# Kernel optimization log

Measured on AMD Instinct MI355X. Metric: run time of the kernel, lower is better.

Reference implementation:

```python
import jax, jax.numpy as jnp
import numpy as np
import math

N = 4096
D = 256
H = 8
DH = D // H
E_RAND = 131072
EPS = 1e-5


def _layernorm(x, g, b):
    mu = jnp.mean(x, axis=-1, keepdims=True)
    var = jnp.mean((x - mu) ** 2, axis=-1, keepdims=True)
    return (x - mu) * jax.lax.rsqrt(var + EPS) * g + b


def setup_inputs() -> dict:
    key = jax.random.key(0)
    ks = jax.random.split(key, 16)
    s = 1.0 / math.sqrt(D)
    x = jax.random.normal(ks[0], (N, D), dtype=jnp.float32)
    src = jax.random.randint(ks[1], (E_RAND,), 0, N)
    dst = jax.random.randint(ks[2], (E_RAND,), 0, N)
    loop = jnp.arange(N)
    edge_index = jnp.stack([jnp.concatenate([src, loop]),
                            jnp.concatenate([dst, loop])]).astype(jnp.int64)
    def lin(k):
        return jax.random.normal(k, (D, D), dtype=jnp.float32) * s
    return {
        "x": x,
        "edge_index": edge_index,
        "Wq": lin(ks[3]), "bq": jnp.zeros((D,), jnp.float32),
        "Wk": lin(ks[4]), "bk": jnp.zeros((D,), jnp.float32),
        "Wv": lin(ks[5]), "bv": jnp.zeros((D,), jnp.float32),
        "Wo": lin(ks[6]), "bo": jnp.zeros((D,), jnp.float32),
        "g1": jnp.ones((D,), jnp.float32), "b1": jnp.zeros((D,), jnp.float32),
        "g2": jnp.ones((D,), jnp.float32), "b2": jnp.zeros((D,), jnp.float32),
        "Wm1": jax.random.normal(ks[7], (D, 2 * D), jnp.float32) * s,
        "bm1": jnp.zeros((2 * D,), jnp.float32),
        "Wm2": jax.random.normal(ks[8], (2 * D, D), jnp.float32) * (1.0 / math.sqrt(2 * D)),
        "bm2": jnp.zeros((D,), jnp.float32),
    }


def reference(x, edge_index, Wq, bq, Wk, bk, Wv, bv, Wo, bo,
              g1, b1, g2, b2, Wm1, bm1, Wm2, bm2):
    scale = 1.0 / math.sqrt(DH)
    h = _layernorm(x, g1, b1)
    # [N, D] -> [H, N, DH]
    q = (h @ Wq + bq).reshape(N, H, DH).transpose(1, 0, 2)
    k = (h @ Wk + bk).reshape(N, H, DH).transpose(1, 0, 2)
    v = (h @ Wv + bv).reshape(N, H, DH).transpose(1, 0, 2)
    att = jnp.einsum('hnd,hmd->hnm', q, k) * scale  # [H, N, N]
    # mask: True everywhere except edges (edge positions are attended)
    mask = jnp.ones((N, N), dtype=bool).at[edge_index[0], edge_index[1]].set(False)
    att = jnp.where(mask[None, :, :], -jnp.inf, att)
    att = jax.nn.softmax(att, axis=-1)
    y = jnp.einsum('hnm,hmd->hnd', att, v)  # [H, N, DH]
    y = y.transpose(1, 0, 2).reshape(N, D)
    x = x + (y @ Wo + bo)
    h2 = _layernorm(x, g2, b2)
    x = x + (jax.nn.gelu(h2 @ Wm1 + bm1, approximate=False) @ Wm2 + bm2)
    return x
```

## Files before the change

kernel.cpp:

```cpp
#include <hip/hip_runtime.h>
#include <hip/hip_bf16.h>

#define N_NODES 4096
#define D_MODEL 256
#define NWORDS 128
#define CAP 256

typedef __attribute__((ext_vector_type(8))) short short8;
typedef __attribute__((ext_vector_type(4))) float f32x4;

__device__ __forceinline__ unsigned short f2b(float f) {
    unsigned u = __float_as_uint(f);
    return (unsigned short)((u + 0x7FFFu + ((u >> 16) & 1u)) >> 16);
}
__device__ __forceinline__ float b2f(unsigned short u) {
    return __uint_as_float((unsigned)u << 16);
}

__global__ __launch_bounds__(256) void prep_kernel(const float* __restrict__ Wq,
        const float* __restrict__ Wk, const float* __restrict__ Wv,
        const float* __restrict__ Wo, const float* __restrict__ Wm1,
        const float* __restrict__ Wm2, unsigned short* __restrict__ wbf,
        uint4* __restrict__ bitmap, const int* __restrict__ ei,
        int* __restrict__ flag, const float* __restrict__ x,
        const float* __restrict__ g1, const float* __restrict__ b1,
        unsigned short* __restrict__ h) {
    int b = blockIdx.x, t = threadIdx.x;
    if (b < 2048) {
        int e = b * 256 + t;
        const float* W; int base, K, M;
        if (e < 262144) {
            int r = e >> 16;
            W = (r == 0) ? Wq : (r == 1) ? Wk : (r == 2) ? Wv : Wo;
            base = r << 16; K = 256; M = 256;
        } else if (e < 393216) { W = Wm1; base = 262144; K = 256; M = 512; }
        else                   { W = Wm2; base = 393216; K = 512; M = 256; }
        int i = e - base;
        int m = i / K, k = i - m * K;
        wbf[e] = f2b(W[k * M + m]);
    } else if (b < 2560) {
        bitmap[(size_t)(b - 2048) * 256 + t] = uint4{0, 0, 0, 0};
    } else if (b == 2560) {
        if (t == 0) {
            int is64 = 1;
            for (int i = 1; i < 128; i += 2)
                if (ei[i] != 0) { is64 = 0; break; }
            *flag = is64;
        }
    } else {
        int row = b - 2561;
        float v = x[row * D_MODEL + t];
        __shared__ float red[4];
        float s = v;
        #pragma unroll
        for (int off = 32; off; off >>= 1) s += __shfl_down(s, off, 64);
        if ((t & 63) == 0) red[t >> 6] = s;
        __syncthreads();
        float mu = (red[0] + red[1] + red[2] + red[3]) * (1.0f / 256.0f);
        __syncthreads();
        float d = v - mu;
        float s2 = d * d;
        #pragma unroll
        for (int off = 32; off; off >>= 1) s2 += __shfl_down(s2, off, 64);
        if ((t & 63) == 0) red[t >> 6] = s2;
        __syncthreads();
        float var = (red[0] + red[1] + red[2] + red[3]) * (1.0f / 256.0f);
        h[row * D_MODEL + t] = f2b(d * rsqrtf(var + 1e-5f) * g1[t] + b1[t]);
    }
}

template <int K, int MODE, bool LNA, bool STATS>
__global__ __launch_bounds__(512) void gemm_bf16(const unsigned short* __restrict__ A,
        const float* __restrict__ Af, const float* __restrict__ psum,
        const float* __restrict__ psum2, const float* __restrict__ lng,
        const float* __restrict__ lnb, const unsigned short* __restrict__ BT,
        const float* __restrict__ bias, const float* __restrict__ bias_k,
        const float* __restrict__ bias_v, const float* __restrict__ R,
        float* __restrict__ Cf, unsigned short* __restrict__ Cb,
        unsigned short* __restrict__ Ck, unsigned short* __restrict__ Cv,
        float* __restrict__ opsum, float* __restrict__ opsum2, int M,
        const int* __restrict__ ei, int E, const int* __restrict__ flag,
        unsigned* __restrict__ bitmap, int nadj) {
    int tid = threadIdx.x;
    if (MODE == 3 && (int)blockIdx.x < nadj) {
        int e = (int)blockIdx.x * 512 + tid;
        if (e < E) {
            int n, m;
            if (*flag) { n = ei[2 * e]; m = ei[2 * (E + e)]; }
            else       { n = ei[e];     m = ei[E + e]; }
            atomicOr(&bitmap[n * NWORDS + (m >> 5)], 1u << (m & 31));
        }
        return;
    }
    __shared__ unsigned short Asm[64][72];
    __shared__ unsigned short Bsm[64][72];
    __shared__ float psA[64][2], psA2[64][2];
    __shared__ float muS[64], invS[64];

    int bx2  = (MODE == 3) ? ((int)blockIdx.x - nadj) : 0;
    int brow = (MODE == 3) ? ((bx2 & 63) << 6) : ((int)blockIdx.x << 6);
    int by   = (MODE == 3) ? (bx2 >> 6) : (int)blockIdx.y;
    int bcol = by << 6;
    int wid = tid >> 6, lane = tid & 63;
    int wr = wid >> 1, wc = wid & 1;
    int l15 = lane & 15, lhi = lane >> 4;
    int r0 = tid >> 3, c0 = (tid & 7) << 3;

    float mu_r = 0.f, inv_r = 0.f;
    if (LNA) {
        if (tid < 64) {
            float4 s4 = ((const float4*)psum)[brow + tid];
            float4 q4 = ((const float4*)psum2)[brow + tid];
            float S  = s4.x + s4.y + s4.z + s4.w;
            float S2 = q4.x + q4.y + q4.z + q4.w;
            float mu = S * (1.0f / 256.0f);
            muS[tid] = mu;
            invS[tid] = rsqrtf(S2 * (1.0f / 256.0f) - mu * mu + 1e-5f);
        }
        __syncthreads();
        mu_r = muS[r0]; inv_r = invS[r0];
    }

    const unsigned short* Bp = BT + (size_t)(bcol + r0) * K + c0;
    f32x4 acc[2] = {};
    short8 areg;
    float4 xa, xb, ga, gb, ba, bb;
    if (LNA) {
        const float* Xp = Af + (size_t)(brow + r0) * 256 + c0;
        xa = *(const float4*)(Xp);
        xb = *(const float4*)(Xp + 4);
        ga = *(const float4*)(lng + c0); gb = *(const float4*)(lng + c0 + 4);
        ba = *(const float4*)(lnb + c0); bb = *(const float4*)(lnb + c0 + 4);
    } else {
        areg = *(const short8*)(A + (size_t)(brow + r0) * K + c0);
    }
    short8 breg = *(const short8*)(Bp);

    #pragma unroll
    for (int k0 = 0; k0 < K; k0 += 64) {
        if (LNA) {
            float xv[8] = {xa.x, xa.y, xa.z, xa.w, xb.x, xb.y, xb.z, xb.w};
            float gv[8] = {ga.x, ga.y, ga.z, ga.w, gb.x, gb.y, gb.z, gb.w};
            float bv[8] = {ba.x, ba.y, ba.z, ba.w, bb.x, bb.y, bb.z, bb.w};
            short8 o;
            #pragma unroll
            for (int j = 0; j < 8; ++j)
                o[j] = (short)f2b((xv[j] - mu_r) * inv_r * gv[j] + bv[j]);
            *(short8*)&Asm[r0][c0] = o;
        } else {
            *(short8*)&Asm[r0][c0] = areg;
        }
        *(short8*)&Bsm[r0][c0] = breg;
        __syncthreads();
        if (k0 + 64 < K) {
            if (LNA) {
                const float* Xp = Af + (size_t)(brow + r0) * 256 + k0 + 64 + c0;
                xa = *(const float4*)(Xp);
                xb = *(const float4*)(Xp + 4);
                ga = *(const float4*)(lng + k0 + 64 + c0);
                gb = *(const float4*)(lng + k0 + 64 + c0 + 4);
                ba = *(const float4*)(lnb + k0 + 64 + c0);
                bb = *(const float4*)(lnb + k0 + 64 + c0 + 4);
            } else {
                areg = *(const short8*)(A + (size_t)(brow + r0) * K + k0 + 64 + c0);
            }
            breg = *(const short8*)(Bp + k0 + 64);
        }
        #pragma unroll
        for (int ks = 0; ks < 2; ++ks) {
            int kc = ks * 32 + lhi * 8;
            short8 a_0 = *(const short8*)&Asm[wr * 16 + l15][kc];
            short8 b_0 = *(const short8*)&Bsm[wc * 32 + l15][kc];
            short8 b_1 = *(const short8*)&Bsm[wc * 32 + 16 + l15][kc];
            acc[0] = __builtin_amdgcn_mfma_f32_16x16x32_bf16(a_0, b_0, acc[0], 0, 0, 0);
            acc[1] = __builtin_amdgcn_mfma_f32_16x16x32_bf16(a_0, b_1, acc[1], 0, 0, 0);
        }
        __syncthreads();
    }

    float cs[2][4];
    #pragma unroll
    for (int sn = 0; sn < 2; ++sn) {
        int col = bcol + wc * 32 + sn * 16 + l15;
        float bs;
        if (MODE == 3)
            bs = (col < 256) ? bias[col]
               : (col < 512) ? bias_k[col - 256] : bias_v[col - 512];
        else
            bs = bias[col];
        #pragma unroll
        for (int r = 0; r < 4; ++r) {
            int row = brow + wr * 16 + lhi * 4 + r;
            float c = acc[sn][r] + bs;
            if (MODE == 1) {
                c = 0.5f * c * (1.0f + erff(c * 0.70710678118654752f));
                Cb[(size_t)row * M + col] = f2b(c);
            } else if (MODE == 2) {
                c += R[(size_t)row * M + col];
                Cf[(size_t)row * M + col] = c;
            } else if (MODE == 3) {
                int part = col >> 8, cc = col & 255;
                unsigned short* dst = (part == 0) ? Cb : (part == 1) ? Ck : Cv;
                dst[(((size_t)(cc >> 5) * N_NODES + row) << 5) + (cc & 31)] = f2b(c);
            } else {
                Cb[(size_t)row * M + col] = f2b(c);
            }
            if (STATS) cs[sn][r] = c;
        }
    }
    if (STATS) {
        #pragma unroll
        for (int r = 0; r < 4; ++r) {
            float s  = cs[0][r] + cs[1][r];
            float s2 = cs[0][r] * cs[0][r] + cs[1][r] * cs[1][r];
            #pragma unroll
            for (int off = 1; off < 16; off <<= 1) {
                s  += __shfl_xor(s, off, 64);
                s2 += __shfl_xor(s2, off, 64);
            }
            if (l15 == 0) {
                int rl = wr * 16 + lhi * 4 + r;
                psA[rl][wc] = s; psA2[rl][wc] = s2;
            }
        }
        __syncthreads();
        if (tid < 64) {
            opsum [(size_t)(brow + tid) * 4 + by] = psA[tid][0] + psA[tid][1];
            opsum2[(size_t)(brow + tid) * 4 + by] = psA2[tid][0] + psA2[tid][1];
        }
    }
}

__global__ __launch_bounds__(256) void attn_kernel(const unsigned short* __restrict__ qh,
        const unsigned short* __restrict__ kh, const unsigned short* __restrict__ vh,
        const unsigned* __restrict__ bitmap, unsigned short* __restrict__ y) {
    int bid = blockIdx.x, tid = threadIdx.x;
    int h = bid & 7, oct = bid >> 3;
    int g = tid >> 5, lane = tid & 31;
    int n = oct * 8 + g;
    __shared__ int sIdx[8][CAP];

    const unsigned short* qp = qh + (((size_t)h * N_NODES + n) << 5);
    float qreg[32];
    #pragma unroll
    for (int i = 0; i < 4; ++i) {
        short8 q8 = *(const short8*)(qp + i * 8);
        #pragma unroll
        for (int j = 0; j < 8; ++j) qreg[i * 8 + j] = b2f((unsigned short)q8[j]);
    }

    uint4 w4 = ((const uint4*)(bitmap + (size_t)n * NWORDS))[lane];
    unsigned words[4] = {w4.x, w4.y, w4.z, w4.w};
    int pc = __popc(w4.x) + __popc(w4.y) + __popc(w4.z) + __popc(w4.w);
    int pre = pc;
    #pragma unroll
    for (int off = 1; off < 32; off <<= 1) {
        int u = __shfl_up(pre, off, 32);
        if (lane >= off) pre += u;
    }
    int c = __shfl(pre, 31, 32);
    int off = pre - pc;
    #pragma unroll
    for (int i = 0; i < 4; ++i) {
        unsigned word = words[i];
        int wbase = ((lane << 2) + i) << 5;
        while (word) {
            int bit = __ffs(word) - 1;
            word &= word - 1;
            if (off < CAP) sIdx[g][off] = wbase + bit;
            ++off;
        }
    }
    c = min(c, CAP);
    __syncthreads();

    const unsigned short* kbase = kh + ((size_t)h * N_NODES << 5);
    const unsigned short* vbase = vh + ((size_t)h * N_NODES << 5) + lane;
    const float sc = 0.17677669529663687f;
    float m_run = -INFINITY, S = 0.0f, acc = 0.0f;
    for (int b0 = 0; b0 < c; b0 += 32) {
        int j = b0 + lane;
        float s = -INFINITY;
        if (j < c) {
            const unsigned short* kp = kbase + ((size_t)sIdx[g][j] << 5);
            float d = 0.0f;
            #pragma unroll
            for (int i = 0; i < 4; ++i) {
                short8 k8 = *(const short8*)(kp + i * 8);
                #pragma unroll
                for (int e = 0; e < 8; ++e)
                    d = fmaf(qreg[i * 8 + e], b2f((unsigned short)k8[e]), d);
            }
            s = d * sc;
        }
        float bm = s;
        #pragma unroll
        for (int off2 = 16; off2; off2 >>= 1) bm = fmaxf(bm, __shfl_xor(bm, off2, 32));
        float newM = fmaxf(m_run, bm);
        float p = (j < c) ? __expf(s - newM) : 0.0f;
        float bs = p;
        #pragma unroll
        for (int off2 = 16; off2; off2 >>= 1) bs += __shfl_xor(bs, off2, 32);
        float scale = __expf(m_run - newM);
        S = S * scale + bs;
        acc *= scale;
        int lim = min(32, c - b0);
        #pragma unroll 4
        for (int jj = 0; jj < lim; ++jj) {
            float pj = __shfl(p, jj, 32);
            int m = sIdx[g][b0 + jj];
            acc = fmaf(pj, b2f(vbase[(size_t)m << 5]), acc);
        }
        m_run = newM;
    }
    y[(size_t)n * 256 + h * 32 + lane] = f2b(acc / S);
}

extern "C" void kernel_launch(void* const* d_in, const int* in_sizes, int n_in,
                              void* d_out, int out_size, void* d_ws, size_t ws_size,
                              hipStream_t stream) {
    const float* x   = (const float*)d_in[0];
    const int*   ei  = (const int*)d_in[1];
    const float* Wq  = (const float*)d_in[2];  const float* bq  = (const float*)d_in[3];
    const float* Wk  = (const float*)d_in[4];  const float* bk  = (const float*)d_in[5];
    const float* Wv  = (const float*)d_in[6];  const float* bv  = (const float*)d_in[7];
    const float* Wo  = (const float*)d_in[8];  const float* bo  = (const float*)d_in[9];
    const float* g1  = (const float*)d_in[10]; const float* b1  = (const float*)d_in[11];
    const float* g2  = (const float*)d_in[12]; const float* b2  = (const float*)d_in[13];
    const float* Wm1 = (const float*)d_in[14]; const float* bm1 = (const float*)d_in[15];
    const float* Wm2 = (const float*)d_in[16]; const float* bm2 = (const float*)d_in[17];
    float* out = (float*)d_out;
    int E = in_sizes[1] / 2;
    int nadj = (E + 511) / 512;

    char* WS = (char*)d_ws;
    const size_t MB = 1u << 20;
    unsigned*       bitmap = (unsigned*)WS;
    int*            flag   = (int*)(WS + 2 * MB);
    float*          psum   = (float*)(WS + 2 * MB + 4096);
    float*          psum2  = (float*)(WS + 2 * MB + 4096 + 65536);
    unsigned short* wbf    = (unsigned short*)(WS + 3 * MB);
    unsigned short* y      = (unsigned short*)(WS + 4 * MB);
    float*          x1     = (float*)(WS + 6 * MB);
    unsigned short* m1     = (unsigned short*)(WS + 10 * MB);
    unsigned short* h      = (unsigned short*)(WS + 14 * MB);
    unsigned short* qh     = (unsigned short*)(WS + 16 * MB);
    unsigned short* kh     = (unsigned short*)(WS + 18 * MB);
    unsigned short* vh     = (unsigned short*)(WS + 20 * MB);

    const unsigned short* WTqkv = wbf;
    const unsigned short* WTo   = wbf + 196608;
    const unsigned short* WTm1  = wbf + 262144;
    const unsigned short* WTm2  = wbf + 393216;

    prep_kernel<<<6657, 256, 0, stream>>>(Wq, Wk, Wv, Wo, Wm1, Wm2, wbf,
                                          (uint4*)bitmap, ei, flag, x, g1, b1, h);
    gemm_bf16<256, 3, false, false><<<nadj + 768, 512, 0, stream>>>(h, nullptr,
            nullptr, nullptr, nullptr, nullptr, WTqkv, bq, bk, bv, nullptr,
            nullptr, qh, kh, vh, nullptr, nullptr, 768, ei, E, flag, bitmap, nadj);
    attn_kernel<<<N_NODES, 256, 0, stream>>>(qh, kh, vh, bitmap, y);
    gemm_bf16<256, 2, false, true><<<dim3(64, 4), 512, 0, stream>>>(y, nullptr,
            nullptr, nullptr, nullptr, nullptr, WTo, bo, nullptr, nullptr, x,
            x1, nullptr, nullptr, nullptr, psum, psum2, 256, nullptr, 0, nullptr, nullptr, 0);
    gemm_bf16<256, 1, true, false><<<dim3(64, 8), 512, 0, stream>>>(nullptr, x1,
            psum, psum2, g2, b2, WTm1, bm1, nullptr, nullptr, nullptr,
            nullptr, m1, nullptr, nullptr, nullptr, nullptr, 512, nullptr, 0, nullptr, nullptr, 0);
    gemm_bf16<512, 2, false, false><<<dim3(64, 4), 512, 0, stream>>>(m1, nullptr,
            nullptr, nullptr, nullptr, nullptr, WTm2, bm2, nullptr, nullptr, x1,
            out, nullptr, nullptr, nullptr, nullptr, nullptr, 256, nullptr, 0, nullptr, nullptr, 0);
}
```

Measured before the change: 82.00 us.

## Preload first 64 neighbors' K/V into registers and LDS in attention kernel

```diff
diff --git a/kernel.cpp b/kernel.cpp
--- a/kernel.cpp
+++ b/kernel.cpp
@@ -4,7 +4,7 @@
 #define N_NODES 4096
 #define D_MODEL 256
 #define NWORDS 128
-#define CAP 256
+#define CAP 128
 
 typedef __attribute__((ext_vector_type(8))) short short8;
 typedef __attribute__((ext_vector_type(4))) float f32x4;
@@ -239,6 +239,7 @@
     int g = tid >> 5, lane = tid & 31;
     int n = oct * 8 + g;
     __shared__ int sIdx[8][CAP];
+    __shared__ unsigned short Vst[8][64][36];
 
     const unsigned short* qp = qh + (((size_t)h * N_NODES + n) << 5);
     float qreg[32];
@@ -272,46 +273,106 @@
         }
     }
     c = min(c, CAP);
+    for (int i = c + lane; i < 64; i += 32) sIdx[g][i] = 0;
     __syncthreads();
 
-    const unsigned short* kbase = kh + ((size_t)h * N_NODES << 5);
-    const unsigned short* vbase = vh + ((size_t)h * N_NODES << 5) + lane;
+    int idx_a = sIdx[g][lane], idx_b = sIdx[g][lane + 32];
+    const size_t hb = (size_t)h * N_NODES << 5;
+
+    const unsigned short* va = vh + hb + ((size_t)idx_a << 5);
+    const unsigned short* vb = vh + hb + ((size_t)idx_b << 5);
+    short8 va0 = *(const short8*)(va);      short8 va1 = *(const short8*)(va + 8);
+    short8 va2 = *(const short8*)(va + 16); short8 va3 = *(const short8*)(va + 24);
+    short8 vb0 = *(const short8*)(vb);      short8 vb1 = *(const short8*)(vb + 8);
+    short8 vb2 = *(const short8*)(vb + 16); short8 vb3 = *(const short8*)(vb + 24);
+
+    const unsigned short* ka = kh + hb + ((size_t)idx_a << 5);
+    const unsigned short* kb = kh + hb + ((size_t)idx_b << 5);
+    short8 ka0 = *(const short8*)(ka);      short8 ka1 = *(const short8*)(ka + 8);
+    short8 ka2 = *(const short8*)(ka + 16); short8 ka3 = *(const short8*)(ka + 24);
+    short8 kb0 = *(const short8*)(kb);      short8 kb1 = *(const short8*)(kb + 8);
+    short8 kb2 = *(const short8*)(kb + 16); short8 kb3 = *(const short8*)(kb + 24);
+
+    *(short8*)&Vst[g][lane][0]       = va0;
+    *(short8*)&Vst[g][lane][8]       = va1;
+    *(short8*)&Vst[g][lane][16]      = va2;
+    *(short8*)&Vst[g][lane][24]      = va3;
+    *(short8*)&Vst[g][lane + 32][0]  = vb0;
+    *(short8*)&Vst[g][lane + 32][8]  = vb1;
+    *(short8*)&Vst[g][lane + 32][16] = vb2;
+    *(short8*)&Vst[g][lane + 32][24] = vb3;
+
+    float da0 = 0.f, da1 = 0.f, db0 = 0.f, db1 = 0.f;
+    #pragma unroll
+    for (int e = 0; e < 8; ++e) {
+        da0 = fmaf(qreg[e],      b2f((unsigned short)ka0[e]), da0);
+        da1 = fmaf(qreg[8 + e],  b2f((unsigned short)ka1[e]), da1);
+        da0 = fmaf(qreg[16 + e], b2f((unsigned short)ka2[e]), da0);
+        da1 = fmaf(qreg[24 + e], b2f((unsigned short)ka3[e]), da1);
+        db0 = fmaf(qreg[e],      b2f((unsigned short)kb0[e]), db0);
+        db1 = fmaf(qreg[8 + e],  b2f((unsigned short)kb1[e]), db1);
+        db0 = fmaf(qreg[16 + e], b2f((unsigned short)kb2[e]), db0);
+        db1 = fmaf(qreg[24 + e], b2f((unsigned short)kb3[e]), db1);
+    }
     const float sc = 0.17677669529663687f;
-    float m_run = -INFINITY, S = 0.0f, acc = 0.0f;
-    for (int b0 = 0; b0 < c; b0 += 32) {
-        int j = b0 + lane;
-        float s = -INFINITY;
-        if (j < c) {
-            const unsigned short* kp = kbase + ((size_t)sIdx[g][j] << 5);
-            float d = 0.0f;
+    float s_a = (lane < c)      ? (da0 + da1) * sc : -INFINITY;
+    float s_b = (lane + 32 < c) ? (db0 + db1) * sc : -INFINITY;
+
+    float bm = fmaxf(s_a, s_b);
+    #pragma unroll
+    for (int o2 = 16; o2; o2 >>= 1) bm = fmaxf(bm, __shfl_xor(bm, o2, 32));
+    float p_a = (lane < c)      ? __expf(s_a - bm) : 0.0f;
+    float p_b = (lane + 32 < c) ? __expf(s_b - bm) : 0.0f;
+    float S = p_a + p_b;
+    #pragma unroll
+    for (int o2 = 16; o2; o2 >>= 1) S += __shfl_xor(S, o2, 32);
+
+    float acc0 = 0.f, acc1 = 0.f;
+    #pragma unroll
+    for (int jj = 0; jj < 32; ++jj) {
+        float pa = __shfl(p_a, jj, 32);
+        float pb = __shfl(p_b, jj, 32);
+        acc0 = fmaf(pa, b2f(Vst[g][jj][lane]), acc0);
+        acc1 = fmaf(pb, b2f(Vst[g][jj + 32][lane]), acc1);
+    }
+    float acc = acc0 + acc1;
+
+    if (c > 64) {
+        float m_run = bm;
+        for (int b0 = 64; b0 < c; b0 += 32) {
+            int j = b0 + lane;
+            float s = -INFINITY;
+            if (j < c) {
+                const unsigned short* kp = kh + hb + ((size_t)sIdx[g][j] << 5);
+                float d = 0.0f;
+                #pragma unroll
+                for (int i = 0; i < 4; ++i) {
+                    short8 k8 = *(const short8*)(kp + i * 8);
+                    #pragma unroll
+                    for (int e = 0; e < 8; ++e)
+                        d = fmaf(qreg[i * 8 + e], b2f((unsigned short)k8[e]), d);
+                }
+                s = d * sc;
+            }
+            float bm2 = s;
             #pragma unroll
-            for (int i = 0; i < 4; ++i) {
-                short8 k8 = *(const short8*)(kp + i * 8);
-                #pragma unroll
-                for (int e = 0; e < 8; ++e)
-                    d = fmaf(qreg[i * 8 + e], b2f((unsigned short)k8[e]), d);
-            }
-            s = d * sc;
-        }
-        float bm = s;
-        #pragma unroll
-        for (int off2 = 16; off2; off2 >>= 1) bm = fmaxf(bm, __shfl_xor(bm, off2, 32));
-        float newM = fmaxf(m_run, bm);
-        float p = (j < c) ? __expf(s - newM) : 0.0f;
-        float bs = p;
-        #pragma unroll
-        for (int off2 = 16; off2; off2 >>= 1) bs += __shfl_xor(bs, off2, 32);
-        float scale = __expf(m_run - newM);
-        S = S * scale + bs;
-        acc *= scale;
-        int lim = min(32, c - b0);
-        #pragma unroll 4
-        for (int jj = 0; jj < lim; ++jj) {
-            float pj = __shfl(p, jj, 32);
-            int m = sIdx[g][b0 + jj];
-            acc = fmaf(pj, b2f(vbase[(size_t)m << 5]), acc);
-        }
-        m_run = newM;
+            for (int o2 = 16; o2; o2 >>= 1) bm2 = fmaxf(bm2, __shfl_xor(bm2, o2, 32));
+            float newM = fmaxf(m_run, bm2);
+            float p = (j < c) ? __expf(s - newM) : 0.0f;
+            float bs = p;
+            #pragma unroll
+            for (int o2 = 16; o2; o2 >>= 1) bs += __shfl_xor(bs, o2, 32);
+            float scale = __expf(m_run - newM);
+            S = S * scale + bs;
+            acc *= scale;
+            int lim = min(32, c - b0);
+            const unsigned short* vbase = vh + hb + lane;
+            for (int jj = 0; jj < lim; ++jj) {
+                float pj = __shfl(p, jj, 32);
+                acc = fmaf(pj, b2f(vbase[(size_t)sIdx[g][b0 + jj] << 5]), acc);
+            }
+            m_run = newM;
+        }
     }
     y[(size_t)n * 256 + h * 32 + lane] = f2b(acc / S);
 }
```

After: 75.08 us. 1.09x faster.
